# Kernel optimization log

Measured on AMD Instinct MI355X. Metric: run time of the kernel, lower is better.

The kernel has to match this reference:

```python
import jax, jax.numpy as jnp
import numpy as np

MODEL_DIM = 1024
NUM_HEADS = 16
HEAD_DIM = MODEL_DIM // NUM_HEADS
B, N = 4, 2048


def setup_inputs() -> dict:
    key = jax.random.key(0)
    ks = jax.random.split(key, 6)
    s = 1.0 / np.sqrt(MODEL_DIM)
    x = jax.random.normal(ks[0], (B, N, MODEL_DIM), dtype=jnp.float32)
    Wq = jax.random.uniform(ks[1], (MODEL_DIM, MODEL_DIM), jnp.float32, -s, s)
    Wk = jax.random.uniform(ks[2], (MODEL_DIM, MODEL_DIM), jnp.float32, -s, s)
    Wv = jax.random.uniform(ks[3], (MODEL_DIM, MODEL_DIM), jnp.float32, -s, s)
    Wo = jax.random.uniform(ks[4], (MODEL_DIM, MODEL_DIM), jnp.float32, -s, s)
    bo = jax.random.uniform(ks[5], (MODEL_DIM,), jnp.float32, -s, s)
    return {"x": x, "Wq": Wq, "Wk": Wk, "Wv": Wv, "Wo": Wo, "bo": bo}


def reference(x, Wq, Wk, Wv, Wo, bo):
    # QKV projections (no bias), split heads: b n (h d) -> b h n d
    def split(t):
        b, n, _ = t.shape
        return t.reshape(b, n, NUM_HEADS, HEAD_DIM).transpose(0, 2, 1, 3)

    q = split(x @ Wq.T)
    k = split(x @ Wk.T)
    v = split(x @ Wv.T)

    scale = HEAD_DIM ** (-0.5)
    scores = jnp.einsum('bhnd,bhmd->bhnm', q, k) * scale  # [B,H,N,N]
    # causal mask (is_causal=True)
    causal = jnp.tril(jnp.ones((N, N), dtype=bool))
    scores = jnp.where(causal, scores, -jnp.inf)
    attn = jax.nn.softmax(scores, axis=-1)
    out = jnp.einsum('bhnm,bhmd->bhnd', attn, v)  # [B,H,N,D]
    out = out.transpose(0, 2, 1, 3).reshape(B, N, MODEL_DIM)
    return out @ Wo.T + bo
```

## Files before the change

### kernel.cpp

```cpp
#include <hip/hip_runtime.h>
#include <hip/hip_bf16.h>

typedef unsigned short u16;
typedef __attribute__((ext_vector_type(8))) __bf16 bf16x8;
typedef __attribute__((ext_vector_type(4))) float f32x4;
typedef __attribute__((ext_vector_type(2))) unsigned int u32x2;

#define MODEL_DIM 1024
#define NUM_HEADS 16
#define HEAD_DIM  64
#define BATCH     4
#define SEQ       2048
#define ROWS      (BATCH*SEQ)

static __device__ __forceinline__ u16 f2bf(float f) {
    union { __hip_bfloat16 h; u16 u; } cv;
    cv.h = __float2bfloat16(f);
    return cv.u;
}

static __device__ __forceinline__ unsigned cvtpk(float lo, float hi) {
    unsigned d;
    asm volatile("v_cvt_pk_bf16_f32 %0, %1, %2" : "=v"(d) : "v"(lo), "v"(hi));
    return d;
}

static __device__ __forceinline__ float max3f(float a, float b, float c) {
    float d;
    asm volatile("v_max3_f32 %0, %1, %2, %3" : "=v"(d) : "v"(a), "v"(b), "v"(c));
    return d;
}

static __device__ __forceinline__ void gload16(const u16* g, unsigned lds_byte) {
    __builtin_amdgcn_global_load_lds(
        (const __attribute__((address_space(1))) unsigned int*)g,
        (__attribute__((address_space(3))) unsigned int*)(uintptr_t)lds_byte,
        16, 0, 0);
}

__global__ void castk_all(const float* __restrict__ x,
                          const float* __restrict__ w0, const float* __restrict__ w1,
                          const float* __restrict__ w2, const float* __restrict__ w3,
                          u16* __restrict__ out) {
    const int total = ROWS * MODEL_DIM + 4 * MODEL_DIM * MODEL_DIM;
    int i = (blockIdx.x * blockDim.x + threadIdx.x) * 4;
    int stride = gridDim.x * blockDim.x * 4;
    for (; i < total; i += stride) {
        const float* src;
        int off;
        if (i < ROWS * MODEL_DIM) { src = x; off = i; }
        else {
            int j = i - ROWS * MODEL_DIM;
            int w = j >> 20;
            off = j & 1048575;
            src = (w == 0) ? w0 : (w == 1) ? w1 : (w == 2) ? w2 : w3;
        }
        float4 v = *reinterpret_cast<const float4*>(src + off);
        ushort4 o;
        o.x = f2bf(v.x); o.y = f2bf(v.y); o.z = f2bf(v.z); o.w = f2bf(v.w);
        *reinterpret_cast<ushort4*>(out + i) = o;
    }
}


static __device__ __forceinline__ bf16x8 frag_read(const char* base, int row, int h,
                                                   int lo, int hi) {
    return *reinterpret_cast<const bf16x8*>(
        base + row * 128 + ((h * 64 + hi * 16) ^ ((lo & 7) << 4)));
}

template<int EPI>
__global__ __launch_bounds__(512, 2) void gemm_pipe(
    const u16* __restrict__ A,
    const u16* __restrict__ Wq, const u16* __restrict__ Wk, const u16* __restrict__ Wv,
    u16* __restrict__ qO, u16* __restrict__ kO, u16* __restrict__ vO,
    float* __restrict__ outF, const float* __restrict__ bias)
{
    __shared__ u16 As[2 * 16384];
    __shared__ u16 Bs[2 * 8192];
    const int t    = threadIdx.x;
    const int wid  = t >> 6;
    const int lane = t & 63;
    const int lo   = lane & 15, hi = lane >> 4;
    const int bm   = blockIdx.x * 256;
    int mat, bn;
    const u16* W;
    u16* outB = nullptr;
    float qscale = 1.0f;
    if (EPI == 0) {
        mat = blockIdx.y >> 3;
        bn  = (blockIdx.y & 7) * 128;
        W   = (mat == 0) ? Wq : (mat == 1) ? Wk : Wv;
        outB = (mat == 0) ? qO : (mat == 1) ? kO : vO;
        qscale = (mat == 0) ? 0.18033688f : 1.0f;
    } else {
        bn = blockIdx.y * 128;
        W  = Wq;
    }
    const int wr = wid >> 1, wc = wid & 1;
    const int K = MODEL_DIM;
    const unsigned AsB = (unsigned)(uintptr_t)As;
    const unsigned BsB = (unsigned)(uintptr_t)Bs;

    const u16* aSrc[4]; unsigned aDst[4];
    const u16* bSrc[2]; unsigned bDst[2];
#pragma unroll
    for (int ti = 0; ti < 4; ti++) {
        int o = t * 8 + ti * 4096;
        int row = o >> 6;
        int colb = ((o & 63) * 2) ^ ((row & 7) << 4);
        aSrc[ti] = A + (size_t)(bm + row) * K + (colb >> 1);
        aDst[ti] = (unsigned)(o * 2);
    }
#pragma unroll
    for (int ti = 0; ti < 2; ti++) {
        int o = t * 8 + ti * 4096;
        int row = o >> 6;
        int colb = ((o & 63) * 2) ^ ((row & 7) << 4);
        bSrc[ti] = W + (size_t)(bn + row) * K + (colb >> 1);
        bDst[ti] = (unsigned)(o * 2);
    }

    f32x4 acc[4][4];
#pragma unroll
    for (int m = 0; m < 4; m++)
#pragma unroll
        for (int n = 0; n < 4; n++) acc[m][n] = (f32x4){0.f, 0.f, 0.f, 0.f};

#pragma unroll
    for (int ti = 0; ti < 4; ti++) gload16(aSrc[ti], AsB + aDst[ti]);
#pragma unroll
    for (int ti = 0; ti < 2; ti++) gload16(bSrc[ti], BsB + bDst[ti]);

    for (int kt = 0; kt < 16; kt++) {
        const int p = kt & 1;
        if (kt < 15) {
            const int ko = (kt + 1) * 64;
            const unsigned pa = (unsigned)((p ^ 1) * 32768);
            const unsigned pb = (unsigned)((p ^ 1) * 16384);
#pragma unroll
            for (int ti = 0; ti < 4; ti++) gload16(aSrc[ti] + ko, AsB + pa + aDst[ti]);
#pragma unroll
            for (int ti = 0; ti < 2; ti++) gload16(bSrc[ti] + ko, BsB + pb + bDst[ti]);
            asm volatile("s_waitcnt vmcnt(6)" ::: "memory");
        } else {
            asm volatile("s_waitcnt vmcnt(0)" ::: "memory");
        }
        __builtin_amdgcn_s_barrier();
        __builtin_amdgcn_sched_barrier(0);

        const char* Ab = (const char*)As + p * 32768;
        const char* Bb = (const char*)Bs + p * 16384;
#pragma unroll
        for (int kk = 0; kk < 2; kk++) {
            bf16x8 bfr[4];
#pragma unroll
            for (int n = 0; n < 4; n++)
                bfr[n] = frag_read(Bb, wc * 64 + n * 16 + lo, kk, lo, hi);
#pragma unroll
            for (int mh = 0; mh < 2; mh++) {
                bf16x8 af[2];
#pragma unroll
                for (int m2 = 0; m2 < 2; m2++)
                    af[m2] = frag_read(Ab, wr * 64 + (mh * 2 + m2) * 16 + lo, kk, lo, hi);
                __builtin_amdgcn_s_setprio(1);
#pragma unroll
                for (int m2 = 0; m2 < 2; m2++)
#pragma unroll
                    for (int n = 0; n < 4; n++)
                        acc[mh * 2 + m2][n] = __builtin_amdgcn_mfma_f32_16x16x32_bf16(af[m2], bfr[n], acc[mh * 2 + m2][n], 0, 0, 0);
                __builtin_amdgcn_s_setprio(0);
            }
        }
    }

#pragma unroll
    for (int m = 0; m < 4; m++)
#pragma unroll
        for (int n = 0; n < 4; n++)
#pragma unroll
            for (int r = 0; r < 4; r++) {
                int row = bm + wr * 64 + m * 16 + hi * 4 + r;
                int col = bn + wc * 64 + n * 16 + lo;
                if (EPI == 0) {
                    int b = row >> 11, np = row & 2047;
                    int hh = col >> 6, dd = col & 63;
                    outB[(((size_t)(b * NUM_HEADS + hh) * SEQ + np) << 6) + dd] = f2bf(acc[m][n][r] * qscale);
                } else {
                    outF[(size_t)row * MODEL_DIM + col] = acc[m][n][r] + bias[col];
                }
            }
}


static __device__ __forceinline__ u32x2 tr16(unsigned int addr) {
    u32x2 r;
    asm volatile("ds_read_b64_tr_b16 %0, %1" : "=v"(r) : "v"(addr));
    return r;
}

__global__ __launch_bounds__(256, 6) void attn(
    const u16* __restrict__ Q,
    const u16* __restrict__ Kg,
    const u16* __restrict__ Vg,
    u16* __restrict__ O)
{
    __shared__ u16 lds[12288];
    const int t    = threadIdx.x;
    const int wid  = t >> 6, lane = t & 63;
    const int lo   = lane & 15, hi = lane >> 4;

    const int g    = blockIdx.x;
    const int slot = g >> 3;
    const int bh   = ((slot & 7) << 3) + (g & 7);
    const int a    = slot >> 3;
    const int kq   = a >> 2, a0 = a & 3;
    const int rk   = 7 - kq;
    const int qt   = 4 * rk + ((rk & 1) ? 3 - a0 : a0);

    const size_t base = (size_t)bh * SEQ * 64;
    const int qbase = qt * 64 + wid * 16;
    const unsigned ldsb = (unsigned)(uintptr_t)lds;

    int srcK[2], srcV[2];
    unsigned dstK[2], dstV[2];
#pragma unroll
    for (int ti = 0; ti < 2; ti++) {
        int o   = t * 8 + ti * 2048;
        int row = o >> 6;
        int colb = ((o & 63) * 2) ^ ((row & 7) << 4);
        srcK[ti] = row * 64 + (colb >> 1);
        dstK[ti] = ldsb + o * 2;
        int st = o >> 9;
        int kv = (st >> 2) * 32 + ((o >> 4) & 31);
        int d  = (st & 3) * 16 + (o & 15);
        srcV[ti] = kv * 64 + d;
        dstV[ti] = ldsb + 16384u + o * 2;
    }

    bf16x8 qf[2];
#pragma unroll
    for (int h = 0; h < 2; h++)
        qf[h] = *reinterpret_cast<const bf16x8*>(Q + base + (size_t)(qbase + lo) * 64 + h * 32 + hi * 8);
    asm volatile("" : "+v"(qf[0]), "+v"(qf[1]));

    bf16x8 ones;
    {
        union { u16 uu[8]; bf16x8 v; } ov;
#pragma unroll
        for (int e = 0; e < 8; e++) ov.uu[e] = 0x3F80;
        ones = ov.v;
    }

    float m_run = -3.0e38f;
    f32x4 acc[4], lacc = (f32x4){0.f, 0.f, 0.f, 0.f};
#pragma unroll
    for (int dt = 0; dt < 4; dt++) acc[dt] = (f32x4){0.f, 0.f, 0.f, 0.f};

    const unsigned vtb = ldsb + 16384u + (unsigned)((hi * 64 + lo * 4) * 2);

    {
        const u16* Kt = Kg + base;
#pragma unroll
        for (int ti = 0; ti < 2; ti++) gload16(Kt + srcK[ti], dstK[ti]);
        asm volatile("s_waitcnt vmcnt(0)" ::: "memory");
    }

    for (int j = 0; j <= qt; j++) {
        const int p = j & 1;
        __builtin_amdgcn_s_barrier();
        {
            const u16* Vt = Vg + base + (size_t)j * 4096;
#pragma unroll
            for (int ti = 0; ti < 2; ti++) gload16(Vt + srcV[ti], dstV[ti]);
            if (j < qt) {
                const u16* Kt = Kg + base + (size_t)(j + 1) * 4096;
                const unsigned bs = (unsigned)((p ^ 1) * 8192);
#pragma unroll
                for (int ti = 0; ti < 2; ti++) gload16(Kt + srcK[ti], dstK[ti] + bs);
            }
        }
        __builtin_amdgcn_sched_barrier(0);

        const char* Kcur = (const char*)lds + p * 8192;
        f32x4 s[4];
#pragma unroll
        for (int kh = 0; kh < 2; kh++) {
            bf16x8 kfa[2][2];
#pragma unroll
            for (int k2 = 0; k2 < 2; k2++)
#pragma unroll
                for (int h = 0; h < 2; h++)
                    kfa[k2][h] = *reinterpret_cast<const bf16x8*>(
                        Kcur + ((kh * 2 + k2) * 16 + lo) * 128 + ((h * 64 + hi * 16) ^ ((lo & 7) << 4)));
            __builtin_amdgcn_s_setprio(1);
#pragma unroll
            for (int k2 = 0; k2 < 2; k2++) {
                f32x4 a2 = (f32x4){0.f, 0.f, 0.f, 0.f};
#pragma unroll
                for (int h = 0; h < 2; h++)
                    a2 = __builtin_amdgcn_mfma_f32_16x16x32_bf16(kfa[k2][h], qf[h], a2, 0, 0, 0);
                s[kh * 2 + k2] = a2;
            }
            __builtin_amdgcn_s_setprio(0);
        }
        if (j == qt) {
            const int ql = wid * 16 + lo;
#pragma unroll
            for (int kt = 0; kt < 4; kt++)
#pragma unroll
                for (int r = 0; r < 4; r++)
                    if (kt * 16 + hi * 4 + r > ql) s[kt][r] = -1.0e30f;
        }
        float t0 = max3f(s[0][0], s[0][1], s[0][2]);
        float t1 = max3f(s[0][3], s[1][0], s[1][1]);
        float t2 = max3f(s[1][2], s[1][3], s[2][0]);
        float t3 = max3f(s[2][1], s[2][2], s[2][3]);
        float t4 = max3f(s[3][0], s[3][1], s[3][2]);
        float u0 = max3f(t0, t1, t2);
        float u1 = max3f(t3, t4, s[3][3]);
        float vm = fmaxf(u0, u1);
        float x16 = __shfl_xor(vm, 16);
        float x32 = __shfl_xor(vm, 32);
        float x48 = __shfl_xor(vm, 48);
        vm = fmaxf(fmaxf(vm, x16), fmaxf(x32, x48));
        if (!__all(vm <= m_run + 8.0f)) {
            float nm = fmaxf(m_run, vm);
            float sc = exp2f(m_run - nm);
            m_run = nm;
            lacc *= sc;
#pragma unroll
            for (int dt = 0; dt < 4; dt++)
#pragma unroll
                for (int r = 0; r < 4; r++) acc[dt][r] *= sc;
        }
#pragma unroll
        for (int kt = 0; kt < 4; kt++)
#pragma unroll
            for (int r = 0; r < 4; r++)
                s[kt][r] = exp2f(s[kt][r] - m_run);
        bf16x8 pa[2];
        {
            union { unsigned w[4]; bf16x8 v; } q0, q1;
            q0.w[0] = cvtpk(s[0][0], s[0][1]);
            q0.w[1] = cvtpk(s[0][2], s[0][3]);
            q0.w[2] = cvtpk(s[1][0], s[1][1]);
            q0.w[3] = cvtpk(s[1][2], s[1][3]);
            q1.w[0] = cvtpk(s[2][0], s[2][1]);
            q1.w[1] = cvtpk(s[2][2], s[2][3]);
            q1.w[2] = cvtpk(s[3][0], s[3][1]);
            q1.w[3] = cvtpk(s[3][2], s[3][3]);
            pa[0] = q0.v;
            pa[1] = q1.v;
        }
        lacc = __builtin_amdgcn_mfma_f32_16x16x32_bf16(ones, pa[0], lacc, 0, 0, 0);
        lacc = __builtin_amdgcn_mfma_f32_16x16x32_bf16(ones, pa[1], lacc, 0, 0, 0);

        if (j < qt) {
            asm volatile("s_waitcnt vmcnt(2)" ::: "memory");
        } else {
            asm volatile("s_waitcnt vmcnt(0)" ::: "memory");
        }
        __builtin_amdgcn_s_barrier();
        __builtin_amdgcn_sched_barrier(0);

#pragma unroll
        for (int pr = 0; pr < 2; pr++) {
            u32x2 tv[2][2][2];
#pragma unroll
            for (int d2 = 0; d2 < 2; d2++)
#pragma unroll
                for (int h = 0; h < 2; h++)
#pragma unroll
                    for (int sel = 0; sel < 2; sel++)
                        tv[d2][h][sel] = tr16(vtb + (unsigned)(((h * 4 + pr * 2 + d2) * 512 + sel * 256) * 2));
            asm volatile("s_waitcnt lgkmcnt(0)" ::: "memory");
            __builtin_amdgcn_sched_barrier(0);
            __builtin_amdgcn_s_setprio(1);
#pragma unroll
            for (int d2 = 0; d2 < 2; d2++) {
#pragma unroll
                for (int h = 0; h < 2; h++) {
                    union { unsigned int w[4]; bf16x8 v; } bv;
                    bv.w[0] = tv[d2][h][0][0];
                    bv.w[1] = tv[d2][h][0][1];
                    bv.w[2] = tv[d2][h][1][0];
                    bv.w[3] = tv[d2][h][1][1];
                    acc[pr * 2 + d2] = __builtin_amdgcn_mfma_f32_16x16x32_bf16(bv.v, pa[h], acc[pr * 2 + d2], 0, 0, 0);
                }
            }
            __builtin_amdgcn_s_setprio(0);
        }
        asm volatile("s_waitcnt vmcnt(0)" ::: "memory");
    }

    const float inv = 1.0f / lacc[0];
    const int b = bh >> 4, hh = bh & 15;
    const size_t orow = ((size_t)(b * SEQ + qbase + lo)) * 1024 + hh * 64;
#pragma unroll
    for (int dt = 0; dt < 4; dt++) {
        union { unsigned w[2]; uint2 d2; } pk;
        pk.w[0] = cvtpk(acc[dt][0] * inv, acc[dt][1] * inv);
        pk.w[1] = cvtpk(acc[dt][2] * inv, acc[dt][3] * inv);
        *reinterpret_cast<uint2*>(O + orow + dt * 16 + hi * 4) = pk.d2;
    }
}

extern "C" void kernel_launch(void* const* d_in, const int* in_sizes, int n_in,
                              void* d_out, int out_size, void* d_ws, size_t ws_size,
                              hipStream_t stream) {
    const float* x  = (const float*)d_in[0];
    const float* Wq = (const float*)d_in[1];
    const float* Wk = (const float*)d_in[2];
    const float* Wv = (const float*)d_in[3];
    const float* Wo = (const float*)d_in[4];
    const float* bo = (const float*)d_in[5];
    float* out = (float*)d_out;

    char* ws = (char*)d_ws;
    u16* xb  = (u16*)ws;
    u16* wqb = (u16*)(ws + 16777216);
    u16* wkb = wqb + 1048576;
    u16* wvb = wkb + 1048576;
    u16* wob = wvb + 1048576;
    u16* q   = (u16*)(ws + 16777216 + 8388608);
    u16* k   = q + 8388608;
    u16* v   = k + 8388608;
    u16* ao  = v + 8388608;

    castk_all<<<3072, 256, 0, stream>>>(x, Wq, Wk, Wv, Wo, xb);

    gemm_pipe<0><<<dim3(ROWS / 256, 24), 512, 0, stream>>>(
        xb, wqb, wkb, wvb, q, k, v, nullptr, nullptr);

    attn<<<2048, 256, 0, stream>>>(q, k, v, ao);

    gemm_pipe<1><<<dim3(ROWS / 256, MODEL_DIM / 128), 512, 0, stream>>>(
        ao, wob, nullptr, nullptr, nullptr, nullptr, nullptr, out, bo);
}
```

Before: 154.5 us.

## Double attention query tile to 128 rows per block, reusing each K/V tile

Each attention block now processes 128 query rows (two 16-row subtiles per wave) instead of 64, so every K/V tile loaded into LDS feeds twice as many MFMAs and total K/V global traffic roughly halves. The grid shrinks to 1024 blocks with a new block-to-(head, query tile) mapping that pairs long and short causal tiles, and subtiles fully past the diagonal skip the QK/softmax work and feed zero probabilities to the PV MFMAs. Launch bounds drop from 6 to 4 blocks per SIMD to make room for the doubled accumulators, which lowers occupancy and may leave fewer blocks in flight to hide latency.

```diff
diff --git a/kernel.cpp b/kernel.cpp
--- a/kernel.cpp
+++ b/kernel.cpp
@@ -199,7 +199,7 @@
     return r;
 }
 
-__global__ __launch_bounds__(256, 6) void attn(
+__global__ __launch_bounds__(256, 4) void attn(
     const u16* __restrict__ Q,
     const u16* __restrict__ Kg,
     const u16* __restrict__ Vg,
@@ -210,16 +210,14 @@
     const int wid  = t >> 6, lane = t & 63;
     const int lo   = lane & 15, hi = lane >> 4;
 
-    const int g    = blockIdx.x;
-    const int slot = g >> 3;
-    const int bh   = ((slot & 7) << 3) + (g & 7);
-    const int a    = slot >> 3;
-    const int kq   = a >> 2, a0 = a & 3;
-    const int rk   = 7 - kq;
-    const int qt   = 4 * rk + ((rk & 1) ? 3 - a0 : a0);
+    const int g  = blockIdx.x;
+    const int u  = g & 255, kk_ = g >> 8;
+    const int bh = ((u >> 5) << 3) + ((u >> 2) & 7);
+    const int rr_ = u & 3;
+    const int qt = (kk_ < 2) ? (15 - 2 * rr_ - kk_) : (2 * rr_ + 3 - kk_);
 
     const size_t base = (size_t)bh * SEQ * 64;
-    const int qbase = qt * 64 + wid * 16;
+    const int qbase = qt * 128 + wid * 32;
     const unsigned ldsb = (unsigned)(uintptr_t)lds;
 
     int srcK[2], srcV[2];
@@ -238,26 +236,34 @@
         dstV[ti] = ldsb + 16384u + o * 2;
     }
 
-    bf16x8 qf[2];
-#pragma unroll
-    for (int h = 0; h < 2; h++)
-        qf[h] = *reinterpret_cast<const bf16x8*>(Q + base + (size_t)(qbase + lo) * 64 + h * 32 + hi * 8);
-    asm volatile("" : "+v"(qf[0]), "+v"(qf[1]));
-
-    bf16x8 ones;
+    bf16x8 qf[2][2];
+#pragma unroll
+    for (int m = 0; m < 2; m++)
+#pragma unroll
+        for (int h = 0; h < 2; h++)
+            qf[m][h] = *reinterpret_cast<const bf16x8*>(
+                Q + base + (size_t)(qbase + m * 16 + lo) * 64 + h * 32 + hi * 8);
+    asm volatile("" : "+v"(qf[0][0]), "+v"(qf[0][1]), "+v"(qf[1][0]), "+v"(qf[1][1]));
+
+    bf16x8 ones, zf;
     {
-        union { u16 uu[8]; bf16x8 v; } ov;
-#pragma unroll
-        for (int e = 0; e < 8; e++) ov.uu[e] = 0x3F80;
-        ones = ov.v;
-    }
-
-    float m_run = -3.0e38f;
-    f32x4 acc[4], lacc = (f32x4){0.f, 0.f, 0.f, 0.f};
-#pragma unroll
-    for (int dt = 0; dt < 4; dt++) acc[dt] = (f32x4){0.f, 0.f, 0.f, 0.f};
+        union { u16 uu[8]; bf16x8 v; } ov, zv;
+#pragma unroll
+        for (int e = 0; e < 8; e++) { ov.uu[e] = 0x3F80; zv.uu[e] = 0; }
+        ones = ov.v; zf = zv.v;
+    }
+
+    float m_run[2] = {-3.0e38f, -3.0e38f};
+    f32x4 acc[2][4], lacc[2];
+#pragma unroll
+    for (int m = 0; m < 2; m++) {
+        lacc[m] = (f32x4){0.f, 0.f, 0.f, 0.f};
+#pragma unroll
+        for (int dt = 0; dt < 4; dt++) acc[m][dt] = (f32x4){0.f, 0.f, 0.f, 0.f};
+    }
 
     const unsigned vtb = ldsb + 16384u + (unsigned)((hi * 64 + lo * 4) * 2);
+    const int jmax = 2 * qt + 1;
 
     {
         const u16* Kt = Kg + base;
@@ -266,14 +272,14 @@
         asm volatile("s_waitcnt vmcnt(0)" ::: "memory");
     }
 
-    for (int j = 0; j <= qt; j++) {
+    for (int j = 0; j <= jmax; j++) {
         const int p = j & 1;
         __builtin_amdgcn_s_barrier();
         {
             const u16* Vt = Vg + base + (size_t)j * 4096;
 #pragma unroll
             for (int ti = 0; ti < 2; ti++) gload16(Vt + srcV[ti], dstV[ti]);
-            if (j < qt) {
+            if (j < jmax) {
                 const u16* Kt = Kg + base + (size_t)(j + 1) * 4096;
                 const unsigned bs = (unsigned)((p ^ 1) * 8192);
 #pragma unroll
@@ -283,80 +289,87 @@
         __builtin_amdgcn_sched_barrier(0);
 
         const char* Kcur = (const char*)lds + p * 8192;
-        f32x4 s[4];
-#pragma unroll
-        for (int kh = 0; kh < 2; kh++) {
-            bf16x8 kfa[2][2];
-#pragma unroll
-            for (int k2 = 0; k2 < 2; k2++)
-#pragma unroll
-                for (int h = 0; h < 2; h++)
-                    kfa[k2][h] = *reinterpret_cast<const bf16x8*>(
-                        Kcur + ((kh * 2 + k2) * 16 + lo) * 128 + ((h * 64 + hi * 16) ^ ((lo & 7) << 4)));
-            __builtin_amdgcn_s_setprio(1);
-#pragma unroll
-            for (int k2 = 0; k2 < 2; k2++) {
-                f32x4 a2 = (f32x4){0.f, 0.f, 0.f, 0.f};
-#pragma unroll
-                for (int h = 0; h < 2; h++)
-                    a2 = __builtin_amdgcn_mfma_f32_16x16x32_bf16(kfa[k2][h], qf[h], a2, 0, 0, 0);
-                s[kh * 2 + k2] = a2;
+        bf16x8 pa[2][2];
+#pragma unroll
+        for (int m = 0; m < 2; m++) {
+            const int band = 2 * qt + ((2 * wid + m) >> 2);
+            if (j <= band) {
+                f32x4 s[4];
+#pragma unroll
+                for (int kh = 0; kh < 2; kh++) {
+                    bf16x8 kfa[2][2];
+#pragma unroll
+                    for (int k2 = 0; k2 < 2; k2++)
+#pragma unroll
+                        for (int h = 0; h < 2; h++)
+                            kfa[k2][h] = *reinterpret_cast<const bf16x8*>(
+                                Kcur + ((kh * 2 + k2) * 16 + lo) * 128 + ((h * 64 + hi * 16) ^ ((lo & 7) << 4)));
+                    __builtin_amdgcn_s_setprio(1);
+#pragma unroll
+                    for (int k2 = 0; k2 < 2; k2++) {
+                        f32x4 a2 = (f32x4){0.f, 0.f, 0.f, 0.f};
+#pragma unroll
+                        for (int h = 0; h < 2; h++)
+                            a2 = __builtin_amdgcn_mfma_f32_16x16x32_bf16(kfa[k2][h], qf[m][h], a2, 0, 0, 0);
+                        s[kh * 2 + k2] = a2;
+                    }
+                    __builtin_amdgcn_s_setprio(0);
+                }
+                if (j == band) {
+                    const int ql = ((2 * wid + m) & 3) * 16 + lo;
+#pragma unroll
+                    for (int kt = 0; kt < 4; kt++)
+#pragma unroll
+                        for (int r = 0; r < 4; r++)
+                            if (kt * 16 + hi * 4 + r > ql) s[kt][r] = -1.0e30f;
+                }
+                float t0 = max3f(s[0][0], s[0][1], s[0][2]);
+                float t1 = max3f(s[0][3], s[1][0], s[1][1]);
+                float t2 = max3f(s[1][2], s[1][3], s[2][0]);
+                float t3 = max3f(s[2][1], s[2][2], s[2][3]);
+                float t4 = max3f(s[3][0], s[3][1], s[3][2]);
+                float u0 = max3f(t0, t1, t2);
+                float u1 = max3f(t3, t4, s[3][3]);
+                float vm = fmaxf(u0, u1);
+                float x16 = __shfl_xor(vm, 16);
+                float x32 = __shfl_xor(vm, 32);
+                float x48 = __shfl_xor(vm, 48);
+                vm = fmaxf(fmaxf(vm, x16), fmaxf(x32, x48));
+                if (!__all(vm <= m_run[m] + 8.0f)) {
+                    float nm = fmaxf(m_run[m], vm);
+                    float sc = exp2f(m_run[m] - nm);
+                    m_run[m] = nm;
+                    lacc[m] *= sc;
+#pragma unroll
+                    for (int dt = 0; dt < 4; dt++)
+#pragma unroll
+                        for (int r = 0; r < 4; r++) acc[m][dt][r] *= sc;
+                }
+#pragma unroll
+                for (int kt = 0; kt < 4; kt++)
+#pragma unroll
+                    for (int r = 0; r < 4; r++)
+                        s[kt][r] = exp2f(s[kt][r] - m_run[m]);
+                union { unsigned w[4]; bf16x8 v; } q0, q1;
+                q0.w[0] = cvtpk(s[0][0], s[0][1]);
+                q0.w[1] = cvtpk(s[0][2], s[0][3]);
+                q0.w[2] = cvtpk(s[1][0], s[1][1]);
+                q0.w[3] = cvtpk(s[1][2], s[1][3]);
+                q1.w[0] = cvtpk(s[2][0], s[2][1]);
+                q1.w[1] = cvtpk(s[2][2], s[2][3]);
+                q1.w[2] = cvtpk(s[3][0], s[3][1]);
+                q1.w[3] = cvtpk(s[3][2], s[3][3]);
+                pa[m][0] = q0.v;
+                pa[m][1] = q1.v;
+                lacc[m] = __builtin_amdgcn_mfma_f32_16x16x32_bf16(ones, pa[m][0], lacc[m], 0, 0, 0);
+                lacc[m] = __builtin_amdgcn_mfma_f32_16x16x32_bf16(ones, pa[m][1], lacc[m], 0, 0, 0);
+            } else {
+                pa[m][0] = zf;
+                pa[m][1] = zf;
             }
-            __builtin_amdgcn_s_setprio(0);
-        }
-        if (j == qt) {
-            const int ql = wid * 16 + lo;
-#pragma unroll
-            for (int kt = 0; kt < 4; kt++)
-#pragma unroll
-                for (int r = 0; r < 4; r++)
-                    if (kt * 16 + hi * 4 + r > ql) s[kt][r] = -1.0e30f;
-        }
-        float t0 = max3f(s[0][0], s[0][1], s[0][2]);
-        float t1 = max3f(s[0][3], s[1][0], s[1][1]);
-        float t2 = max3f(s[1][2], s[1][3], s[2][0]);
-        float t3 = max3f(s[2][1], s[2][2], s[2][3]);
-        float t4 = max3f(s[3][0], s[3][1], s[3][2]);
-        float u0 = max3f(t0, t1, t2);
-        float u1 = max3f(t3, t4, s[3][3]);
-        float vm = fmaxf(u0, u1);
-        float x16 = __shfl_xor(vm, 16);
-        float x32 = __shfl_xor(vm, 32);
-        float x48 = __shfl_xor(vm, 48);
-        vm = fmaxf(fmaxf(vm, x16), fmaxf(x32, x48));
-        if (!__all(vm <= m_run + 8.0f)) {
-            float nm = fmaxf(m_run, vm);
-            float sc = exp2f(m_run - nm);
-            m_run = nm;
-            lacc *= sc;
-#pragma unroll
-            for (int dt = 0; dt < 4; dt++)
-#pragma unroll
-                for (int r = 0; r < 4; r++) acc[dt][r] *= sc;
-        }
-#pragma unroll
-        for (int kt = 0; kt < 4; kt++)
-#pragma unroll
-            for (int r = 0; r < 4; r++)
-                s[kt][r] = exp2f(s[kt][r] - m_run);
-        bf16x8 pa[2];
-        {
-            union { unsigned w[4]; bf16x8 v; } q0, q1;
-            q0.w[0] = cvtpk(s[0][0], s[0][1]);
-            q0.w[1] = cvtpk(s[0][2], s[0][3]);
-            q0.w[2] = cvtpk(s[1][0], s[1][1]);
-            q0.w[3] = cvtpk(s[1][2], s[1][3]);
-            q1.w[0] = cvtpk(s[2][0], s[2][1]);
-            q1.w[1] = cvtpk(s[2][2], s[2][3]);
-            q1.w[2] = cvtpk(s[3][0], s[3][1]);
-            q1.w[3] = cvtpk(s[3][2], s[3][3]);
-            pa[0] = q0.v;
-            pa[1] = q1.v;
-        }
-        lacc = __builtin_amdgcn_mfma_f32_16x16x32_bf16(ones, pa[0], lacc, 0, 0, 0);
-        lacc = __builtin_amdgcn_mfma_f32_16x16x32_bf16(ones, pa[1], lacc, 0, 0, 0);
-
-        if (j < qt) {
+        }
+
+        if (j < jmax) {
             asm volatile("s_waitcnt vmcnt(2)" ::: "memory");
         } else {
             asm volatile("s_waitcnt vmcnt(0)" ::: "memory");
@@ -386,7 +399,9 @@
                     bv.w[1] = tv[d2][h][0][1];
                     bv.w[2] = tv[d2][h][1][0];
                     bv.w[3] = tv[d2][h][1][1];
-                    acc[pr * 2 + d2] = __builtin_amdgcn_mfma_f32_16x16x32_bf16(bv.v, pa[h], acc[pr * 2 + d2], 0, 0, 0);
+#pragma unroll
+                    for (int m = 0; m < 2; m++)
+                        acc[m][pr * 2 + d2] = __builtin_amdgcn_mfma_f32_16x16x32_bf16(bv.v, pa[m][h], acc[m][pr * 2 + d2], 0, 0, 0);
                 }
             }
             __builtin_amdgcn_s_setprio(0);
@@ -394,15 +409,18 @@
         asm volatile("s_waitcnt vmcnt(0)" ::: "memory");
     }
 
-    const float inv = 1.0f / lacc[0];
     const int b = bh >> 4, hh = bh & 15;
-    const size_t orow = ((size_t)(b * SEQ + qbase + lo)) * 1024 + hh * 64;
-#pragma unroll
-    for (int dt = 0; dt < 4; dt++) {
-        union { unsigned w[2]; uint2 d2; } pk;
-        pk.w[0] = cvtpk(acc[dt][0] * inv, acc[dt][1] * inv);
-        pk.w[1] = cvtpk(acc[dt][2] * inv, acc[dt][3] * inv);
-        *reinterpret_cast<uint2*>(O + orow + dt * 16 + hi * 4) = pk.d2;
+#pragma unroll
+    for (int m = 0; m < 2; m++) {
+        const float inv = 1.0f / lacc[m][0];
+        const size_t orow = ((size_t)(b * SEQ + qbase + m * 16 + lo)) * 1024 + hh * 64;
+#pragma unroll
+        for (int dt = 0; dt < 4; dt++) {
+            union { unsigned w[2]; uint2 d2; } pk;
+            pk.w[0] = cvtpk(acc[m][dt][0] * inv, acc[m][dt][1] * inv);
+            pk.w[1] = cvtpk(acc[m][dt][2] * inv, acc[m][dt][3] * inv);
+            *reinterpret_cast<uint2*>(O + orow + dt * 16 + hi * 4) = pk.d2;
+        }
     }
 }
 
@@ -433,7 +451,7 @@
     gemm_pipe<0><<<dim3(ROWS / 256, 24), 512, 0, stream>>>(
         xb, wqb, wkb, wvb, q, k, v, nullptr, nullptr);
 
-    attn<<<2048, 256, 0, stream>>>(q, k, v, ao);
+    attn<<<1024, 256, 0, stream>>>(q, k, v, ao);
 
     gemm_pipe<1><<<dim3(ROWS / 256, MODEL_DIM / 128), 512, 0, stream>>>(
         ao, wob, nullptr, nullptr, nullptr, nullptr, nullptr, out, bo);
```

New measurement: 161.3 us. 1.04x slower.
